# Performance work log

Measured on AMD Instinct MI355X. Metric: run time of the kernel, lower is better.

## Reference

```python
import jax, jax.numpy as jnp
import numpy as np

N_CLASSES = 19


def setup_inputs() -> dict:
    key = jax.random.key(0)
    k1, k2 = jax.random.split(key)
    embedding = jax.random.normal(k1, (4, 32, 128, 128), dtype=jnp.float32)
    label = jax.random.randint(k2, (4, 512, 512), 0, N_CLASSES, dtype=jnp.int64)
    return {"embedding": embedding, "label": label}


def _discriminative_loss(embedding, label, n_classes=N_CLASSES):
    N, H, W = label.shape
    C = embedding.shape[1]
    # bilinear upsample embedding to label resolution (F.upsample mode='bilinear')
    emb = jax.image.resize(embedding, (N, C, H, W), method="bilinear")
    HW = H * W
    emb = emb.reshape(N, C, HW).transpose(0, 2, 1)          # (N, HW, C)
    lab = label.reshape(N, HW)                               # (N, HW)

    onehot = jax.nn.one_hot(lab, n_classes, dtype=emb.dtype)  # (N, HW, K)
    count = onehot.sum(1)                                    # (N, K)
    mask = (count > 0).astype(emb.dtype)                     # (N, K)

    # per-class embedding sum and (biased, /(count+1)) mean
    cls_sum = jnp.einsum("npc,npk->nkc", emb, onehot)       # (N, K, C)
    cls_mean = cls_sum / (count[:, :, None] + 1.0)           # (N, K, C)

    # intra-class: per-pixel squared distance to own-class mean, mean over C
    mean_pp = jnp.take_along_axis(cls_mean, lab[:, :, None], axis=1)  # (N, HW, C)
    d2 = jnp.mean((emb - mean_pp) ** 2, axis=-1)             # (N, HW)
    intra_per_cls = jnp.einsum("np,npk->nk", d2, onehot) / (count + 1.0)  # (N, K)
    n_fg = mask[:, 1:].sum(1)                                # (N,)
    l2_intra = (intra_per_cls[:, 1:] * mask[:, 1:]).sum(1) / n_fg  # (N,)

    # inter-class: pairwise mean squared distance between class means
    diff = cls_mean[:, :, None, :] - cls_mean[:, None, :, :]  # (N, K, K, C)
    inter = jnp.mean(diff ** 2, axis=-1)                     # (N, K, K)
    inter = inter * mask[:, None, :] * mask[:, :, None]
    l2_inter = inter[:, 1:, 1:].reshape(N, -1).sum(1) / (n_fg * n_fg)  # (N,)

    return l2_intra - l2_inter


def reference(embedding, label):
    return _discriminative_loss(embedding, label)
```

## Files before the change

### kernel.cpp

```cpp
#include <hip/hip_runtime.h>

#define NIMG 4
#define NCLS 19
#define CCH  32
#define LH   128
#define LW   128
#define HH   512
#define WW   512
#define HWQ  (LH*LW)
#define HWP  (HH*WW)

#define TR 8
#define TC 8
#define NTX (LW/TC)
#define NTY (LH/TR)
#define NTILE (NTY*NTX)
#define TCELLS (TR*TC)
#define RW 10
#define RING 100
#define NACC (NCLS*CCH)

__device__ __forceinline__ void taps(int v, int lim, int& i0, float& w0, float& w1) {
    int r = v & 3;
    int b = (v >> 2) + ((r < 2) ? -1 : 0);
    float f = 0.125f + 0.25f * (float)((r + 2) & 3);
    w0 = 1.f - f; w1 = f;
    if (b < 0)           { b = 0;       w0 = 1.f; w1 = 0.f; }
    else if (b >= lim)   { b = lim - 1; w0 = 0.f; w1 = 1.f; }
    i0 = b;
}

__global__ __launch_bounds__(256) void k_gram(const float* __restrict__ E,
        float* __restrict__ G, double* __restrict__ AccS, double* __restrict__ AccS2,
        float* __restrict__ AccC, unsigned int* __restrict__ Cnt) {
    int n = blockIdx.y, rp = blockIdx.x;
    int tid = threadIdx.x;
    if (n == 0 && rp == 0) {
        for (int i = tid; i < NIMG * NACC; i += 256) AccS[i] = 0.0;
        if (tid < NIMG * NCLS) { AccS2[tid] = 0.0; AccC[tid] = 0.f; }
        if (tid < NIMG) Cnt[tid] = 0u;
    }
    int x = tid & 127, dy = tid >> 7;
    int y = rp * 2 + dy;
    int yn = (y < LH - 1) ? y + 1 : y;
    int xn = (x < LW - 1) ? x + 1 : x;
    bool fix = ((x & 63) == 63);
    const float* base = E + (size_t)n * CCH * HWQ;
    const float* Ea = base + y * LW + x;
    const float* Eb = base + yn * LW + x;
    const float* Eax = base + y * LW + xn;
    const float* Ebx = base + yn * LW + xn;
    float gs = 0.f, gh = 0.f, gv = 0.f, gda = 0.f;
#pragma unroll 8
    for (int c = 0; c < CCH; c++) {
        float a = Ea[(size_t)c * HWQ];
        float b = Eb[(size_t)c * HWQ];
        float ar = __shfl_down(a, 1);
        float br = __shfl_down(b, 1);
        if (fix) { ar = Eax[(size_t)c * HWQ]; br = Ebx[(size_t)c * HWQ]; }
        gs = fmaf(a, a, gs);
        gh = fmaf(a, ar, gh);
        gv = fmaf(a, b, gv);
        gda = fmaf(a, br, fmaf(ar, b, gda));
    }
    float* Gp = G + (size_t)n * 4 * HWQ + y * LW + x;
    Gp[0] = gs; Gp[HWQ] = gh; Gp[2 * HWQ] = gv; Gp[3 * HWQ] = gda;
}

__global__ __launch_bounds__(256) void k_field(const float* __restrict__ E,
        const int* __restrict__ lab, const float* __restrict__ G,
        double* __restrict__ AccS, double* __restrict__ AccS2,
        float* __restrict__ AccC, unsigned int* __restrict__ Cnt,
        float* __restrict__ out) {
    int tile = blockIdx.x, n = blockIdx.y;
    int ty = tile >> 4, tx = tile & 15;
    int Y0 = ty * TR, X0 = tx * TC;
    __shared__ float A[TCELLS * NCLS];
    __shared__ float Gt[4 * RING];
    __shared__ float red[8 * NCLS * 33];
    __shared__ float S2w[4 * NCLS];
    __shared__ float tmpc[NCLS * 8];
    __shared__ unsigned int sdone;
    __shared__ double cs_d[NCLS * 33];
    __shared__ double m_d[NCLS * 33];
    __shared__ double cnt_d[NCLS], s2_d[NCLS];
    __shared__ double wpart[4];
    __shared__ double sIntra, sNfg;
    int tid = threadIdx.x;

    for (int i = tid; i < TCELLS * NCLS; i += 256) A[i] = 0.f;
    if (tid < 4 * NCLS) S2w[tid] = 0.f;
    const float* Gn = G + (size_t)n * 4 * HWQ;
    for (int i = tid; i < 4 * RING; i += 256) {
        int p = i / RING, r = i - p * RING;
        int gy = r / RW, gx = r - gy * RW;
        int yy = Y0 - 1 + gy; yy = yy < 0 ? 0 : (yy > LH - 1 ? LH - 1 : yy);
        int xx = X0 - 1 + gx; xx = xx < 0 ? 0 : (xx > LW - 1 ? LW - 1 : xx);
        Gt[i] = Gn[(size_t)p * HWQ + yy * LW + xx];
    }
    __syncthreads();

    const float* Gs_ = Gt, *Gh_ = Gt + RING, *Gv_ = Gt + 2 * RING, *Gda_ = Gt + 3 * RING;
    const int* ln = lab + (size_t)n * HWP;
    int h_lo = Y0 * 4 - 2;
    for (int i = tid; i < 36 * RW; i += 256) {
        int hr = i / RW, qi = i - hr * RW;
        int h = h_lo + hr;
        int q = X0 - 1 + qi;
        if (h < 0 || h >= HH || q < 0 || q >= LW) continue;
        int y0; float wy0, wy1;
        taps(h, LH - 1, y0, wy0, wy1);
        int ry = y0 - Y0;
        bool r0 = (unsigned)ry < (unsigned)TR, r1 = (unsigned)(ry + 1) < (unsigned)TR;
        int rxm = q - 1 - X0, rx0 = q - X0, rxp = q + 1 - X0;
        bool bm = (unsigned)rxm < (unsigned)TC, b0 = (unsigned)rx0 < (unsigned)TC,
             bp = (unsigned)rxp < (unsigned)TC;
        int4 l4 = *(const int4*)(ln + h * WW + (q << 2));
        bool fast = (q >= 1) && (q <= 126);
        bool owned = ((unsigned)(h - Y0 * 4) < 32u) && b0;

        if (fast) {
            if (r0) {
                int rb = (ry * TC) * NCLS;
                if (bm) { float* a = &A[rb + rxm * NCLS];
                    atomicAdd(a + l4.x, wy0 * 0.375f); atomicAdd(a + l4.y, wy0 * 0.125f); }
                if (b0) { float* a = &A[rb + rx0 * NCLS];
                    atomicAdd(a + l4.x, wy0 * 0.625f); atomicAdd(a + l4.y, wy0 * 0.875f);
                    atomicAdd(a + l4.z, wy0 * 0.875f); atomicAdd(a + l4.w, wy0 * 0.625f); }
                if (bp) { float* a = &A[rb + rxp * NCLS];
                    atomicAdd(a + l4.z, wy0 * 0.125f); atomicAdd(a + l4.w, wy0 * 0.375f); }
            }
            if (r1) {
                int rb = ((ry + 1) * TC) * NCLS;
                if (bm) { float* a = &A[rb + rxm * NCLS];
                    atomicAdd(a + l4.x, wy1 * 0.375f); atomicAdd(a + l4.y, wy1 * 0.125f); }
                if (b0) { float* a = &A[rb + rx0 * NCLS];
                    atomicAdd(a + l4.x, wy1 * 0.625f); atomicAdd(a + l4.y, wy1 * 0.875f);
                    atomicAdd(a + l4.z, wy1 * 0.875f); atomicAdd(a + l4.w, wy1 * 0.625f); }
                if (bp) { float* a = &A[rb + rxp * NCLS];
                    atomicAdd(a + l4.z, wy1 * 0.125f); atomicAdd(a + l4.w, wy1 * 0.375f); }
            }
            if (owned) {
                float u0 = wy0 * wy0, u1 = wy1 * wy1, u2t = 2.f * wy0 * wy1;
                int g00 = (y0 - Y0 + 1) * RW + rx0;
                float C0 = u0 * Gs_[g00]     + u1 * Gs_[g00 + RW]     + u2t * Gv_[g00];
                float C1 = u0 * Gs_[g00 + 1] + u1 * Gs_[g00 + RW + 1] + u2t * Gv_[g00 + 1];
                float C2 = u0 * Gs_[g00 + 2] + u1 * Gs_[g00 + RW + 2] + u2t * Gv_[g00 + 2];
                float D0 = 2.f * (u0 * Gh_[g00]     + u1 * Gh_[g00 + RW])     + u2t * Gda_[g00];
                float D1 = 2.f * (u0 * Gh_[g00 + 1] + u1 * Gh_[g00 + RW + 1]) + u2t * Gda_[g00 + 1];
                float d2a = fmaf(0.140625f, C0, fmaf(0.390625f, C1, 0.46875f * D0));
                float d2b = fmaf(0.015625f, C0, fmaf(0.765625f, C1, 0.21875f * D0));
                float d2c = fmaf(0.765625f, C1, fmaf(0.015625f, C2, 0.21875f * D1));
                float d2d = fmaf(0.390625f, C1, fmaf(0.140625f, C2, 0.46875f * D1));
                int wv = (tid >> 6) * NCLS;
                atomicAdd(&S2w[wv + l4.x], d2a); atomicAdd(&S2w[wv + l4.y], d2b);
                atomicAdd(&S2w[wv + l4.z], d2c); atomicAdd(&S2w[wv + l4.w], d2d);
            }
        } else {
            int Ls[4] = {l4.x, l4.y, l4.z, l4.w};
            float u0 = wy0 * wy0, u1 = wy1 * wy1, u2t = 2.f * wy0 * wy1;
            int gyr = y0 - Y0 + 1;
            int wv = (tid >> 6) * NCLS;
#pragma unroll
            for (int j = 0; j < 4; j++) {
                int w = (q << 2) + j;
                int x0; float wx0, wx1;
                taps(w, LW - 1, x0, wx0, wx1);
                int rxa = x0 - X0, rxb = rxa + 1;
                int L = Ls[j];
                if (r0) {
                    int rb = (ry * TC) * NCLS;
                    if ((unsigned)rxa < (unsigned)TC) atomicAdd(&A[rb + rxa * NCLS + L], wy0 * wx0);
                    if ((unsigned)rxb < (unsigned)TC) atomicAdd(&A[rb + rxb * NCLS + L], wy0 * wx1);
                }
                if (r1) {
                    int rb = ((ry + 1) * TC) * NCLS;
                    if ((unsigned)rxa < (unsigned)TC) atomicAdd(&A[rb + rxa * NCLS + L], wy1 * wx0);
                    if ((unsigned)rxb < (unsigned)TC) atomicAdd(&A[rb + rxb * NCLS + L], wy1 * wx1);
                }
                if (owned) {
                    int gg = gyr * RW + (x0 - X0 + 1);
                    float Ca = u0 * Gs_[gg]     + u1 * Gs_[gg + RW]     + u2t * Gv_[gg];
                    float Cb = u0 * Gs_[gg + 1] + u1 * Gs_[gg + RW + 1] + u2t * Gv_[gg + 1];
                    float Dd = 2.f * (u0 * Gh_[gg] + u1 * Gh_[gg + RW]) + u2t * Gda_[gg];
                    float d2 = wx0 * wx0 * Ca + wx1 * wx1 * Cb + 2.f * wx0 * wx1 * Dd;
                    atomicAdd(&S2w[wv + L], d2);
                }
            }
        }
    }
    __syncthreads();

    {
        int c = tid >> 3, cy = tid & 7;
        const float* Er = E + ((size_t)n * CCH + c) * HWQ + (Y0 + cy) * LW + X0;
        float4 v0 = *(const float4*)Er;
        float4 v1 = *(const float4*)(Er + 4);
        float ev[8] = {v0.x, v0.y, v0.z, v0.w, v1.x, v1.y, v1.z, v1.w};
        float acc[NCLS];
#pragma unroll
        for (int k = 0; k < NCLS; k++) acc[k] = 0.f;
#pragma unroll
        for (int cx = 0; cx < 8; cx++) {
            const float* Ar = &A[(cy * 8 + cx) * NCLS];
            float e = ev[cx];
#pragma unroll
            for (int k = 0; k < NCLS; k++) acc[k] = fmaf(Ar[k], e, acc[k]);
        }
#pragma unroll
        for (int k = 0; k < NCLS; k++) red[(cy * NCLS + k) * 33 + c] = acc[k];
    }
    if (tid < 8 * NCLS) {
        int g8 = tid / NCLS, k = tid - g8 * NCLS;
        float s = 0.f;
#pragma unroll
        for (int j = 0; j < 8; j++) s += A[(g8 * 8 + j) * NCLS + k];
        tmpc[k * 8 + g8] = s;
    }
    __syncthreads();

    for (int idx = tid; idx < NACC; idx += 256) {
        int k = idx >> 5, c = idx & 31;
        float s = 0.f;
#pragma unroll
        for (int gg = 0; gg < 8; gg++) s += red[(gg * NCLS + k) * 33 + c];
        atomicAdd(&AccS[n * NACC + idx], (double)s);
    }
    if (tid < NCLS) {
        float s = 0.f;
#pragma unroll
        for (int g8 = 0; g8 < 8; g8++) s += tmpc[tid * 8 + g8];
        atomicAdd(&AccC[n * NCLS + tid], s);
        float s2 = S2w[tid] + S2w[NCLS + tid] + S2w[2 * NCLS + tid] + S2w[3 * NCLS + tid];
        atomicAdd(&AccS2[n * NCLS + tid], (double)s2);
    }
    __syncthreads();
    if (tid == 0) { __threadfence(); sdone = atomicAdd(&Cnt[n], 1u); }
    __syncthreads();
    if (sdone != NTILE - 1) return;

    __threadfence();
    for (int idx = tid; idx < NACC; idx += 256)
        cs_d[(idx >> 5) * 33 + (idx & 31)] = atomicAdd(&AccS[n * NACC + idx], 0.0);
    if (tid < NCLS) {
        cnt_d[tid] = (double)atomicAdd(&AccC[n * NCLS + tid], 0.f);
        s2_d[tid]  = atomicAdd(&AccS2[n * NCLS + tid], 0.0);
    }
    __syncthreads();
    for (int idx = tid; idx < NACC; idx += 256) {
        int k = idx >> 5, c = idx & 31;
        m_d[k * 33 + c] = cs_d[k * 33 + c] / (cnt_d[k] + 1.0);
    }
    __syncthreads();
    double vi = 0.0, fg = 0.0;
    if (tid >= 1 && tid < NCLS && cnt_d[tid] > 0.0) {
        fg = 1.0;
        double dot = 0.0, mm = 0.0;
        for (int c = 0; c < CCH; c++) {
            double mv = m_d[tid * 33 + c];
            dot += mv * cs_d[tid * 33 + c];
            mm += mv * mv;
        }
        vi = (s2_d[tid] - 2.0 * dot + cnt_d[tid] * mm) * 0.03125 / (cnt_d[tid] + 1.0);
    }
    if (tid < 64) {
#pragma unroll
        for (int s_ = 32; s_ >= 1; s_ >>= 1) { vi += __shfl_xor(vi, s_); fg += __shfl_xor(fg, s_); }
        if (tid == 0) { sIntra = vi; sNfg = fg; }
    }
    double ve = 0.0;
    for (int t2 = tid; t2 < 324; t2 += 256) {
        int j = 1 + t2 / 18, k = 1 + t2 % 18;
        if (cnt_d[j] > 0.0 && cnt_d[k] > 0.0) {
            double s = 0.0;
            for (int c = 0; c < CCH; c++) {
                double d = m_d[j * 33 + c] - m_d[k * 33 + c];
                s += d * d;
            }
            ve += s * 0.03125;
        }
    }
#pragma unroll
    for (int s_ = 32; s_ >= 1; s_ >>= 1) ve += __shfl_xor(ve, s_);
    if ((tid & 63) == 0) wpart[tid >> 6] = ve;
    __syncthreads();
    if (tid == 0) {
        double inter = wpart[0] + wpart[1] + wpart[2] + wpart[3];
        out[n] = (float)(sIntra / sNfg - inter / (sNfg * sNfg));
    }
}

extern "C" void kernel_launch(void* const* d_in, const int* in_sizes, int n_in,
                              void* d_out, int out_size, void* d_ws, size_t ws_size,
                              hipStream_t stream) {
    const float* E = (const float*)d_in[0];
    const int* lab = (const int*)d_in[1];
    float* out = (float*)d_out;

    double* AccS  = (double*)d_ws;
    double* AccS2 = AccS + (size_t)NIMG * NACC;
    float*  AccC  = (float*)(AccS2 + NIMG * NCLS);
    unsigned int* Cnt = (unsigned int*)(AccC + NIMG * NCLS);
    float*  G     = (float*)(Cnt + NIMG);

    k_gram <<<dim3(64, NIMG),    dim3(256), 0, stream>>>(E, G, AccS, AccS2, AccC, Cnt);
    k_field<<<dim3(NTILE, NIMG), dim3(256), 0, stream>>>(E, lab, G, AccS, AccS2, AccC, Cnt, out);
}
```

Baseline: 139.0 us.

## Replace global double atomics and last-block reduction with per-tile partials and final kernel

Each tile now reduces its per-class embedding sums across lanes with shuffles and writes them to a per-tile partial buffer, replacing the 608 double atomicAdds per block and the shared-memory reduction array. A separate final kernel sums the partials and computes the loss, which removes the last-block counter and threadfence pattern. The label, embedding and Gram-ring loads are hoisted to the start of the block so their latency overlaps, and launch bounds request higher occupancy. The cost is an extra kernel launch and a final reduction done by only four blocks, each reading a 256-entry partial array per slot serially.

```diff
diff --git a/kernel.cpp b/kernel.cpp
--- a/kernel.cpp
+++ b/kernel.cpp
@@ -13,12 +13,11 @@
 #define TR 8
 #define TC 8
 #define NTX (LW/TC)
-#define NTY (LH/TR)
-#define NTILE (NTY*NTX)
+#define NTILE (256)
 #define TCELLS (TR*TC)
 #define RW 10
 #define RING 100
-#define NACC (NCLS*CCH)
+#define NSLOT 608
 
 __device__ __forceinline__ void taps(int v, int lim, int& i0, float& w0, float& w1) {
     int r = v & 3;
@@ -30,16 +29,19 @@
     i0 = b;
 }
 
+__device__ __forceinline__ float ring_fetch(const float* Gn, int i, int Y0, int X0) {
+    int p = i / RING, r = i - p * RING;
+    int gy = r / RW, gx = r - gy * RW;
+    int yy = Y0 - 1 + gy; yy = yy < 0 ? 0 : (yy > LH - 1 ? LH - 1 : yy);
+    int xx = X0 - 1 + gx; xx = xx < 0 ? 0 : (xx > LW - 1 ? LW - 1 : xx);
+    return Gn[(size_t)p * HWQ + yy * LW + xx];
+}
+
 __global__ __launch_bounds__(256) void k_gram(const float* __restrict__ E,
-        float* __restrict__ G, double* __restrict__ AccS, double* __restrict__ AccS2,
-        float* __restrict__ AccC, unsigned int* __restrict__ Cnt) {
+        float* __restrict__ G, float* __restrict__ AccCS) {
     int n = blockIdx.y, rp = blockIdx.x;
     int tid = threadIdx.x;
-    if (n == 0 && rp == 0) {
-        for (int i = tid; i < NIMG * NACC; i += 256) AccS[i] = 0.0;
-        if (tid < NIMG * NCLS) { AccS2[tid] = 0.0; AccC[tid] = 0.f; }
-        if (tid < NIMG) Cnt[tid] = 0u;
-    }
+    if (n == 0 && rp == 0 && tid < NIMG * 2 * NCLS) AccCS[tid] = 0.f;
     int x = tid & 127, dy = tid >> 7;
     int y = rp * 2 + dy;
     int yn = (y < LH - 1) ? y + 1 : y;
@@ -67,47 +69,56 @@
     Gp[0] = gs; Gp[HWQ] = gh; Gp[2 * HWQ] = gv; Gp[3 * HWQ] = gda;
 }
 
-__global__ __launch_bounds__(256) void k_field(const float* __restrict__ E,
+__global__ __launch_bounds__(256, 4) void k_field(const float* __restrict__ E,
         const int* __restrict__ lab, const float* __restrict__ G,
-        double* __restrict__ AccS, double* __restrict__ AccS2,
-        float* __restrict__ AccC, unsigned int* __restrict__ Cnt,
-        float* __restrict__ out) {
+        float* __restrict__ P_sumT, float* __restrict__ AccCS) {
     int tile = blockIdx.x, n = blockIdx.y;
     int ty = tile >> 4, tx = tile & 15;
     int Y0 = ty * TR, X0 = tx * TC;
     __shared__ float A[TCELLS * NCLS];
     __shared__ float Gt[4 * RING];
-    __shared__ float red[8 * NCLS * 33];
     __shared__ float S2w[4 * NCLS];
     __shared__ float tmpc[NCLS * 8];
-    __shared__ unsigned int sdone;
-    __shared__ double cs_d[NCLS * 33];
-    __shared__ double m_d[NCLS * 33];
-    __shared__ double cnt_d[NCLS], s2_d[NCLS];
-    __shared__ double wpart[4];
-    __shared__ double sIntra, sNfg;
     int tid = threadIdx.x;
+    const int* ln = lab + (size_t)n * HWP;
+    int h_lo = Y0 * 4 - 2;
+
+    int hA, qA, hB = 0, qB = 0; bool vB;
+    int4 LA, LB = make_int4(0, 0, 0, 0);
+    {
+        int hr = tid / RW, qi = tid - hr * RW;
+        hA = h_lo + hr; qA = X0 - 1 + qi;
+        int hc = hA < 0 ? 0 : (hA > HH - 1 ? HH - 1 : hA);
+        int qc = qA < 0 ? 0 : (qA > LW - 1 ? LW - 1 : qA);
+        LA = *(const int4*)(ln + hc * WW + (qc << 2));
+    }
+    vB = (tid < 360 - 256);
+    if (vB) {
+        int i = tid + 256;
+        int hr = i / RW, qi = i - hr * RW;
+        hB = h_lo + hr; qB = X0 - 1 + qi;
+        int hc = hB < 0 ? 0 : (hB > HH - 1 ? HH - 1 : hB);
+        int qc = qB < 0 ? 0 : (qB > LW - 1 ? LW - 1 : qB);
+        LB = *(const int4*)(ln + hc * WW + (qc << 2));
+    }
+    int cc = tid >> 3, cy = tid & 7;
+    const float* Er = E + ((size_t)n * CCH + cc) * HWQ + (Y0 + cy) * LW + X0;
+    float4 ev0 = *(const float4*)Er;
+    float4 ev1 = *(const float4*)(Er + 4);
+    const float* Gn = G + (size_t)n * 4 * HWQ;
+    float rv0 = ring_fetch(Gn, tid, Y0, X0);
+    bool rB = (tid < 4 * RING - 256);
+    float rv1 = rB ? ring_fetch(Gn, tid + 256, Y0, X0) : 0.f;
 
     for (int i = tid; i < TCELLS * NCLS; i += 256) A[i] = 0.f;
     if (tid < 4 * NCLS) S2w[tid] = 0.f;
-    const float* Gn = G + (size_t)n * 4 * HWQ;
-    for (int i = tid; i < 4 * RING; i += 256) {
-        int p = i / RING, r = i - p * RING;
-        int gy = r / RW, gx = r - gy * RW;
-        int yy = Y0 - 1 + gy; yy = yy < 0 ? 0 : (yy > LH - 1 ? LH - 1 : yy);
-        int xx = X0 - 1 + gx; xx = xx < 0 ? 0 : (xx > LW - 1 ? LW - 1 : xx);
-        Gt[i] = Gn[(size_t)p * HWQ + yy * LW + xx];
-    }
+    Gt[tid] = rv0;
+    if (rB) Gt[tid + 256] = rv1;
     __syncthreads();
 
     const float* Gs_ = Gt, *Gh_ = Gt + RING, *Gv_ = Gt + 2 * RING, *Gda_ = Gt + 3 * RING;
-    const int* ln = lab + (size_t)n * HWP;
-    int h_lo = Y0 * 4 - 2;
-    for (int i = tid; i < 36 * RW; i += 256) {
-        int hr = i / RW, qi = i - hr * RW;
-        int h = h_lo + hr;
-        int q = X0 - 1 + qi;
-        if (h < 0 || h >= HH || q < 0 || q >= LW) continue;
+    auto process = [&](int h, int q, int4 l4) {
+        if (h < 0 || h >= HH || q < 0 || q >= LW) return;
         int y0; float wy0, wy1;
         taps(h, LH - 1, y0, wy0, wy1);
         int ry = y0 - Y0;
@@ -115,10 +126,8 @@
         int rxm = q - 1 - X0, rx0 = q - X0, rxp = q + 1 - X0;
         bool bm = (unsigned)rxm < (unsigned)TC, b0 = (unsigned)rx0 < (unsigned)TC,
              bp = (unsigned)rxp < (unsigned)TC;
-        int4 l4 = *(const int4*)(ln + h * WW + (q << 2));
         bool fast = (q >= 1) && (q <= 126);
         bool owned = ((unsigned)(h - Y0 * 4) < 32u) && b0;
-
         if (fast) {
             if (r0) {
                 int rb = (ry * TC) * NCLS;
@@ -188,15 +197,13 @@
                 }
             }
         }
-    }
+    };
+    process(hA, qA, LA);
+    if (vB) process(hB, qB, LB);
     __syncthreads();
 
     {
-        int c = tid >> 3, cy = tid & 7;
-        const float* Er = E + ((size_t)n * CCH + c) * HWQ + (Y0 + cy) * LW + X0;
-        float4 v0 = *(const float4*)Er;
-        float4 v1 = *(const float4*)(Er + 4);
-        float ev[8] = {v0.x, v0.y, v0.z, v0.w, v1.x, v1.y, v1.z, v1.w};
+        float ev[8] = {ev0.x, ev0.y, ev0.z, ev0.w, ev1.x, ev1.y, ev1.z, ev1.w};
         float acc[NCLS];
 #pragma unroll
         for (int k = 0; k < NCLS; k++) acc[k] = 0.f;
@@ -208,7 +215,16 @@
             for (int k = 0; k < NCLS; k++) acc[k] = fmaf(Ar[k], e, acc[k]);
         }
 #pragma unroll
-        for (int k = 0; k < NCLS; k++) red[(cy * NCLS + k) * 33 + c] = acc[k];
+        for (int k = 0; k < NCLS; k++) {
+            acc[k] += __shfl_xor(acc[k], 1);
+            acc[k] += __shfl_xor(acc[k], 2);
+            acc[k] += __shfl_xor(acc[k], 4);
+        }
+        if (cy == 0) {
+            float* pt = P_sumT + ((size_t)n * NSLOT + cc) * NTILE + tile;
+#pragma unroll
+            for (int k = 0; k < NCLS; k++) pt[(size_t)k * 32 * NTILE] = acc[k];
+        }
     }
     if (tid < 8 * NCLS) {
         int g8 = tid / NCLS, k = tid - g8 * NCLS;
@@ -218,36 +234,41 @@
         tmpc[k * 8 + g8] = s;
     }
     __syncthreads();
-
-    for (int idx = tid; idx < NACC; idx += 256) {
-        int k = idx >> 5, c = idx & 31;
-        float s = 0.f;
-#pragma unroll
-        for (int gg = 0; gg < 8; gg++) s += red[(gg * NCLS + k) * 33 + c];
-        atomicAdd(&AccS[n * NACC + idx], (double)s);
-    }
     if (tid < NCLS) {
         float s = 0.f;
 #pragma unroll
         for (int g8 = 0; g8 < 8; g8++) s += tmpc[tid * 8 + g8];
-        atomicAdd(&AccC[n * NCLS + tid], s);
+        atomicAdd(&AccCS[n * 2 * NCLS + tid], s);
         float s2 = S2w[tid] + S2w[NCLS + tid] + S2w[2 * NCLS + tid] + S2w[3 * NCLS + tid];
-        atomicAdd(&AccS2[n * NCLS + tid], (double)s2);
-    }
-    __syncthreads();
-    if (tid == 0) { __threadfence(); sdone = atomicAdd(&Cnt[n], 1u); }
-    __syncthreads();
-    if (sdone != NTILE - 1) return;
-
-    __threadfence();
-    for (int idx = tid; idx < NACC; idx += 256)
-        cs_d[(idx >> 5) * 33 + (idx & 31)] = atomicAdd(&AccS[n * NACC + idx], 0.0);
+        atomicAdd(&AccCS[n * 2 * NCLS + NCLS + tid], s2);
+    }
+}
+
+__global__ __launch_bounds__(256) void k_final(const float* __restrict__ P_sumT,
+        const float* __restrict__ AccCS, float* __restrict__ out) {
+    int n = blockIdx.x, tid = threadIdx.x;
+    __shared__ double cs_d[NCLS * 33];
+    __shared__ double m_d[NCLS * 33];
+    __shared__ double cnt_d[NCLS], s2_d[NCLS];
+    __shared__ double wpart[4];
+    __shared__ double sIntra, sNfg;
+
+    for (int idx = tid; idx < NSLOT; idx += 256) {
+        const float4* p4 = (const float4*)(P_sumT + ((size_t)n * NSLOT + idx) * NTILE);
+        double s = 0.0;
+#pragma unroll 4
+        for (int j = 0; j < NTILE / 4; j++) {
+            float4 v = p4[j];
+            s += (double)((v.x + v.y) + (v.z + v.w));
+        }
+        cs_d[(idx >> 5) * 33 + (idx & 31)] = s;
+    }
     if (tid < NCLS) {
-        cnt_d[tid] = (double)atomicAdd(&AccC[n * NCLS + tid], 0.f);
-        s2_d[tid]  = atomicAdd(&AccS2[n * NCLS + tid], 0.0);
-    }
-    __syncthreads();
-    for (int idx = tid; idx < NACC; idx += 256) {
+        cnt_d[tid] = (double)AccCS[n * 2 * NCLS + tid];
+        s2_d[tid]  = (double)AccCS[n * 2 * NCLS + NCLS + tid];
+    }
+    __syncthreads();
+    for (int idx = tid; idx < NSLOT; idx += 256) {
         int k = idx >> 5, c = idx & 31;
         m_d[k * 33 + c] = cs_d[k * 33 + c] / (cnt_d[k] + 1.0);
     }
@@ -297,12 +318,11 @@
     const int* lab = (const int*)d_in[1];
     float* out = (float*)d_out;
 
-    double* AccS  = (double*)d_ws;
-    double* AccS2 = AccS + (size_t)NIMG * NACC;
-    float*  AccC  = (float*)(AccS2 + NIMG * NCLS);
-    unsigned int* Cnt = (unsigned int*)(AccC + NIMG * NCLS);
-    float*  G     = (float*)(Cnt + NIMG);
-
-    k_gram <<<dim3(64, NIMG),    dim3(256), 0, stream>>>(E, G, AccS, AccS2, AccC, Cnt);
-    k_field<<<dim3(NTILE, NIMG), dim3(256), 0, stream>>>(E, lab, G, AccS, AccS2, AccC, Cnt, out);
-}
+    float* P_sumT = (float*)d_ws;
+    float* AccCS  = P_sumT + (size_t)NIMG * NSLOT * NTILE;
+    float* G      = AccCS + NIMG * 2 * NCLS;
+
+    k_gram <<<dim3(64, NIMG),    dim3(256), 0, stream>>>(E, G, AccCS);
+    k_field<<<dim3(NTILE, NIMG), dim3(256), 0, stream>>>(E, lab, G, P_sumT, AccCS);
+    k_final<<<dim3(NIMG),        dim3(256), 0, stream>>>(P_sumT, AccCS, out);
+}
```

Result: slower. 143.1 us (+3.0%).
